# Kernel tuning notes

Hardware: AMD Instinct MI355X
Metric: run time of the kernel (lower is better)

The kernel has to match this reference:

```python
import jax, jax.numpy as jnp
import numpy as np

DIM = 2048
HEADS = 16
HEAD_DIM = DIM // HEADS
B, S = 2, 2048


def setup_inputs() -> dict:
    key = jax.random.key(0)
    k1, k2, k3 = jax.random.split(key, 3)
    x = jax.random.normal(k1, (B, S, DIM), dtype=jnp.float32)
    # causal mask (True = keep), realistic production usage of masked_fill(mask==0,...)
    mask = jnp.tril(jnp.ones((S, S), dtype=bool))
    scale = 1.0 / np.sqrt(DIM)
    W_qkv = jax.random.normal(k2, (DIM, 3 * DIM), dtype=jnp.float32) * scale
    b_qkv = jnp.zeros((3 * DIM,), dtype=jnp.float32)
    W_out = jax.random.normal(k3, (DIM, DIM), dtype=jnp.float32) * scale
    b_out = jnp.zeros((DIM,), dtype=jnp.float32)
    return {"x": x, "mask": mask, "W_qkv": W_qkv, "b_qkv": b_qkv,
            "W_out": W_out, "b_out": b_out}


def reference(x, mask, W_qkv, b_qkv, W_out, b_out):
    b, s, d = x.shape
    # fused QKV projection: [b,s,3d]
    qkv = jnp.einsum('bsd,de->bse', x, W_qkv) + b_qkv
    # [b, s, h, 3*hd] -> [b, h, s, 3*hd] -> chunk into q,k,v
    qkv = qkv.reshape(b, s, HEADS, 3 * HEAD_DIM).transpose(0, 2, 1, 3)
    q, k, v = jnp.split(qkv, 3, axis=-1)  # each [b,h,s,hd]
    scores = jnp.einsum('bhqd,bhkd->bhqk', q, k) / np.sqrt(HEAD_DIM)
    scores = jnp.where(mask, scores, jnp.float32(-1e9))
    attn = jax.nn.softmax(scores, axis=-1)
    # dropout_rate = 0.0 (eval) -> identity
    out = jnp.einsum('bhqk,bhkd->bhqd', attn, v)  # [b,h,s,hd]
    out = out.transpose(0, 2, 1, 3).reshape(b, s, d)
    return jnp.einsum('bsd,de->bse', out, W_out) + b_out
```

## Files before the change

kernel.cpp:

```cpp
#include <hip/hip_runtime.h>
#include <hip/hip_bf16.h>

#define SEQ   2048
#define DIMSZ 2048
#define NHEAD 16
#define HD    128
#define KDIM  2048

typedef __attribute__((ext_vector_type(8))) short bf16x8;
typedef __attribute__((ext_vector_type(4))) float f32x4;
typedef __attribute__((ext_vector_type(4))) short short4v;
typedef __attribute__((ext_vector_type(4))) float float4v;

__device__ __forceinline__ short f2bf(float f) {
    union { __hip_bfloat16 h; short s; } u;
    u.h = __float2bfloat16(f);
    return u.s;
}

__device__ __forceinline__ unsigned pack_bf2(float lo, float hi) {
    return (unsigned)(unsigned short)f2bf(lo) | ((unsigned)(unsigned short)f2bf(hi) << 16);
}

__device__ __forceinline__ void gload_lds16(const void* g, void* l) {
    __builtin_amdgcn_global_load_lds(
        (const __attribute__((address_space(1))) void*)g,
        (__attribute__((address_space(3))) void*)l, 16, 0, 0);
}

__global__ __launch_bounds__(256) void fused_prep(const float* __restrict__ x,
                                                  short* __restrict__ x_bf,
                                                  const float* __restrict__ W_qkv,
                                                  short* __restrict__ wqkv_t,
                                                  const float* __restrict__ W_out,
                                                  short* __restrict__ wout_t) {
    __shared__ float tile[32][33];
    const int bid = blockIdx.x, tid = threadIdx.x;
    if (bid < 8192) {
        int i = (bid * 256 + tid) * 4;
        float4v v = *reinterpret_cast<const float4v*>(x + i);
        short4v o;
        o[0] = f2bf(v[0]); o[1] = f2bf(v[1]); o[2] = f2bf(v[2]); o[3] = f2bf(v[3]);
        *reinterpret_cast<short4v*>(x_bf + i) = o;
        return;
    }
    const float* in;
    short* out;
    int R, C, c0, r0;
    if (bid < 20480) {
        int tb = bid - 8192;
        in = W_qkv; out = wqkv_t; R = 2048; C = 6144;
        c0 = (tb % 192) * 32; r0 = (tb / 192) * 32;
    } else {
        int tb = bid - 20480;
        in = W_out; out = wout_t; R = 2048; C = 2048;
        c0 = (tb % 64) * 32; r0 = (tb / 64) * 32;
    }
    const int tx = tid & 31, ty = tid >> 5;
#pragma unroll
    for (int i = 0; i < 32; i += 8)
        tile[ty + i][tx] = in[(long)(r0 + ty + i) * C + c0 + tx];
    __syncthreads();
#pragma unroll
    for (int i = 0; i < 32; i += 8)
        out[(long)(c0 + ty + i) * R + r0 + tx] = f2bf(tile[tx][ty + i]);
}

template <int MODE, int BM, int BN, int WMC, int WNC>
__global__ __launch_bounds__(512, 2) void gemm8p(const short* __restrict__ A,
                                                 const short* __restrict__ Bt,
                                                 const float* __restrict__ bias,
                                                 float* __restrict__ outf,
                                                 short* __restrict__ q_buf,
                                                 short* __restrict__ k_buf,
                                                 short* __restrict__ vt_buf,
                                                 int ntx) {
    constexpr int QMW = (BM / 2) / WMC;
    constexpr int QNW = (BN / 2) / WNC;
    constexpr int MA = QMW / 16;
    constexpr int NB = QNW / 16;
    constexpr int UA = BM / 64, UB = BN / 64, UT = UA + UB;
    constexpr int RA = MA * 2, RB = NB * 2;
    constexpr int BH0C = (BN / 2 + 63) / 64;
    constexpr int NE = UA / 2 + BH0C, NL = UT - NE;
    constexpr int S0 = 2, S2 = 2;
    constexpr int VM0 = NE + S0;
    constexpr int VM2 = NL + S2;
    constexpr int VM3 = (NE - S2) + NE;
    constexpr int NT = KDIM / 64;

    __shared__ __align__(16) short Alds[2][BM * 64];
    __shared__ __align__(16) short Blds[2][BN * 64];

    const int tid = threadIdx.x;
    const int wv = tid >> 6, ln = tid & 63;
    const int lr = ln & 15, lg = ln >> 4;
    const int wm = wv / WNC, wn = wv % WNC;
    const int q8 = gridDim.x >> 3;
    const int id = blockIdx.x;
    const int swz = (id & 7) * q8 + (id >> 3);
    const int m0 = (swz / ntx) * BM, n0 = (swz % ntx) * BN;

    const int r_l = wv * 8 + (ln >> 3);
    const int g8 = ((ln & 7) ^ ((ln >> 3) & 7)) << 3;

#define STAGE_U(u, bufi, TT)                                                   \
    {                                                                          \
        const bool isA_ = (u) < UA / 2 || (u) >= UA / 2 + UB;                  \
        const int idx_ = (u) < UA / 2 ? (u)                                    \
                         : ((u) < UA / 2 + UB ? (u) - UA / 2 : (u) - UB);      \
        if (isA_)                                                              \
            gload_lds16(A + (long)(m0 + idx_ * 64 + r_l) * KDIM + (TT)*64 + g8,\
                        &Alds[bufi][idx_ * 4096 + wv * 512]);                  \
        else                                                                   \
            gload_lds16(Bt + (long)(n0 + idx_ * 64 + r_l) * KDIM + (TT)*64 + g8,\
                        &Blds[bufi][idx_ * 4096 + wv * 512]);                  \
    }

#define RD(L_, row_, kk_) \
    (*reinterpret_cast<const bf16x8*>(&(L_)[(row_)*64 + ((((kk_)*4 + lg) ^ ((row_)&7)) << 3)]))

#define RD_A(bufi, mh, bank)                                                   \
    _Pragma("unroll") for (int mi = 0; mi < MA; ++mi) {                        \
        int r_ = (mh) * (BM / 2) + wm * QMW + mi * 16 + lr;                    \
        bank[mi][0] = RD(Alds[bufi], r_, 0);                                   \
        bank[mi][1] = RD(Alds[bufi], r_, 1);                                   \
    }
#define RD_B(bufi, nh, bank)                                                   \
    _Pragma("unroll") for (int ni = 0; ni < NB; ++ni) {                        \
        int r_ = (nh) * (BN / 2) + wn * QNW + ni * 16 + lr;                    \
        bank[ni][0] = RD(Blds[bufi], r_, 0);                                   \
        bank[ni][1] = RD(Blds[bufi], r_, 1);                                   \
    }

#define MFMA_Q(qi, AB, BB)                                                     \
    __builtin_amdgcn_s_setprio(1);                                             \
    _Pragma("unroll") for (int kk = 0; kk < 2; ++kk)                           \
        _Pragma("unroll") for (int mi = 0; mi < MA; ++mi)                      \
            _Pragma("unroll") for (int ni = 0; ni < NB; ++ni)                  \
                acc[qi][mi][ni] = __builtin_amdgcn_mfma_f32_16x16x32_bf16(     \
                    AB[mi][kk], BB[ni][kk], acc[qi][mi][ni], 0, 0, 0);         \
    __builtin_amdgcn_s_setprio(0);

#define LGKM(n)                                                                \
    asm volatile("s_waitcnt lgkmcnt(%0)" ::"i"(n) : "memory");                 \
    __builtin_amdgcn_sched_barrier(0);
#define VMC(n) asm volatile("s_waitcnt vmcnt(%0)" ::"i"(n) : "memory");
#define BAR()                                                                  \
    __builtin_amdgcn_s_barrier();                                              \
    __builtin_amdgcn_sched_barrier(0);

    f32x4 acc[4][MA][NB] = {};
    bf16x8 aF0[MA][2], aF1[MA][2], bF0a[NB][2], bF0b[NB][2], bF1[NB][2];

#pragma unroll
    for (int u = 0; u < UT; ++u) STAGE_U(u, 0, 0);
#pragma unroll
    for (int u = 0; u < NE; ++u) STAGE_U(u, 1, 1);
    VMC(NE);
    BAR();
    RD_A(0, 0, aF0);
    RD_B(0, 0, bF0a);

#define TILE_BODY(PAR, T_, BF0C, BF0N)                                         \
    {                                                                          \
        constexpr int cur = PAR, nxt = PAR ^ 1;                                \
        RD_B(cur, 1, bF1);                                                     \
        if ((T_) + 1 < NT) {                                                   \
            STAGE_U(NE + 0, nxt, (T_) + 1);                                    \
            STAGE_U(NE + 1, nxt, (T_) + 1);                                    \
        }                                                                      \
        LGKM(RB);                                                              \
        MFMA_Q(0, aF0, BF0C);                                                  \
        VMC(VM0);                                                              \
        BAR();                                                                 \
        RD_A(cur, 1, aF1);                                                     \
        if ((T_) + 1 < NT) {                                                   \
            _Pragma("unroll") for (int u = NE + S0; u < UT; ++u)               \
                STAGE_U(u, nxt, (T_) + 1);                                     \
        }                                                                      \
        LGKM(RA);                                                              \
        MFMA_Q(1, aF0, bF1);                                                   \
        BAR();                                                                 \
        if ((T_) + 2 < NT) {                                                   \
            STAGE_U(0, cur, (T_) + 2);                                         \
            STAGE_U(1, cur, (T_) + 2);                                         \
        }                                                                      \
        LGKM(0);                                                               \
        MFMA_Q(2, aF1, bF1);                                                   \
        if ((T_) + 2 < NT) { VMC(VM2); } else { VMC(NL); }                     \
        BAR();                                                                 \
        if ((T_) + 1 < NT) {                                                   \
            RD_A(nxt, 0, aF0);                                                 \
            RD_B(nxt, 0, BF0N);                                                \
        }                                                                      \
        if ((T_) + 2 < NT) {                                                   \
            _Pragma("unroll") for (int u = S2; u < NE; ++u)                    \
                STAGE_U(u, cur, (T_) + 2);                                     \
        }                                                                      \
        LGKM(RA + RB);                                                         \
        MFMA_Q(3, aF1, BF0C);                                                  \
        if ((T_) + 2 < NT) { VMC(VM3); } else { VMC(0); }                      \
        BAR();                                                                 \
    }

    for (int TT = 0; TT < NT; TT += 2) {
        TILE_BODY(0, TT, bF0a, bF0b);
        TILE_BODY(1, TT + 1, bF0b, bF0a);
    }

    const int MH[4] = {0, 0, 1, 1}, NHq[4] = {0, 1, 1, 0};
#pragma unroll
    for (int q = 0; q < 4; ++q) {
#pragma unroll
        for (int mi = 0; mi < MA; ++mi) {
#pragma unroll
            for (int ni = 0; ni < NB; ++ni) {
                int col = n0 + NHq[q] * (BN / 2) + wn * QNW + ni * 16 + lr;
                float bv = bias[col];
#pragma unroll
                for (int j = 0; j < 4; ++j) {
                    int row = m0 + MH[q] * (BM / 2) + wm * QMW + mi * 16 + lg * 4 + j;
                    float v = acc[q][mi][ni][j] + bv;
                    if (MODE == 0) {
                        int h = col / (3 * HD);
                        int jj = col - h * (3 * HD);
                        int b = row >> 11, s = row & 2047;
                        int bh = b * NHEAD + h;
                        short sv = f2bf(v);
                        if (jj < HD)
                            q_buf[(bh * SEQ + s) * HD + jj] = sv;
                        else if (jj < 2 * HD)
                            k_buf[(bh * SEQ + s) * HD + (jj - HD)] = sv;
                        else
                            vt_buf[(bh * HD + (jj - 2 * HD)) * SEQ + s] = sv;
                    } else {
                        outf[(long)row * DIMSZ + col] = v;
                    }
                }
            }
        }
    }
#undef STAGE_U
#undef RD
#undef RD_A
#undef RD_B
#undef MFMA_Q
#undef LGKM
#undef VMC
#undef BAR
#undef TILE_BODY
}

__global__ __launch_bounds__(256, 2) void attn_kernel(const short* __restrict__ q_buf,
                                                      const short* __restrict__ k_buf,
                                                      const short* __restrict__ vt_buf,
                                                      short* __restrict__ ao) {
    __shared__ __align__(16) short Klds[2][64 * 128];
    __shared__ __align__(16) short Vlds[2][128 * 64];
    const int tid = threadIdx.x;
    const int wave = tid >> 6, lane = tid & 63;
    const int lr = lane & 15, lg = lane >> 4;
    const int bx = blockIdx.x;
    const int g = bx >> 5;
    const int qt = (g < 8) ? (15 - g) : (g - 8);
    const int bh = bx & 31;
    const int b = bh >> 4, h = bh & 15;
    const int qbase = qt * 128 + wave * 32;
    const float c2 = 0.12752775f;

    bf16x8 qf[2][4];
    {
        const short* qrow = q_buf + ((long)(bh * SEQ + qbase + lr)) * HD;
#pragma unroll
        for (int mi = 0; mi < 2; ++mi)
#pragma unroll
            for (int c = 0; c < 4; ++c)
                qf[mi][c] = *reinterpret_cast<const bf16x8*>(
                    qrow + mi * 16 * HD + c * 32 + lg * 8);
    }
    asm volatile("s_waitcnt vmcnt(0)" ::: "memory");

    const char* kbase = (const char*)(k_buf + (long)bh * SEQ * HD);
    const char* vbase = (const char*)(vt_buf + (long)bh * HD * SEQ);
    const int krow_l = wave * 4 + (lane >> 4);
    const int kcol_l = ((lane & 15) * 16) ^ ((krow_l & 7) << 4);
    const int vrow_l = wave * 8 + (lane >> 3);
    const int vcol_l = ((lane & 7) * 16) ^ ((vrow_l & 7) << 4);

    const int nt = 2 * (qt + 1);
    auto stage = [&](int bufi, int t) {
        const char* ks = kbase + (long)t * 16384 + (long)krow_l * 256 + kcol_l;
        const char* vs = vbase + (long)t * 128 + (long)vrow_l * (SEQ * 2) + vcol_l;
        short* kd = &Klds[bufi][wave * 512];
        short* vd = &Vlds[bufi][wave * 512];
#pragma unroll
        for (int i = 0; i < 4; ++i) {
            gload_lds16(ks + i * 4096, kd + i * 2048);
            gload_lds16(vs + (long)i * 32 * SEQ * 2, vd + i * 2048);
        }
    };

    f32x4 o_acc[2][8] = {};
    float mrow[2] = {-1e30f, -1e30f}, lrow[2] = {0.f, 0.f};

    const int s0 = (lane & 15) | ((lane & 16) << 1);
    const int s1 = s0 + 16;
    const bool hi_ni = (lane & 32) != 0;

    stage(0, 0);
    for (int t = 0; t < nt; ++t) {
        const int cur = t & 1;
        if (t + 1 < nt) {
            stage(cur ^ 1, t + 1);
            asm volatile("s_waitcnt vmcnt(8)" ::: "memory");
        } else {
            asm volatile("s_waitcnt vmcnt(0)" ::: "memory");
        }
        __builtin_amdgcn_s_barrier();
        __builtin_amdgcn_sched_barrier(0);

        const int kv0 = t * 64;
        if (kv0 <= qbase + 31) {
            const short* kl = &Klds[cur][0];
            const short* vl = &Vlds[cur][0];
            bf16x8 kf[4][4];
#pragma unroll
            for (int c = 0; c < 4; ++c)
#pragma unroll
                for (int ni = 0; ni < 4; ++ni)
                    kf[c][ni] = *reinterpret_cast<const bf16x8*>(
                        kl + (((ni * 16 + lr) * 256 +
                               ((c * 64 + lg * 16) ^ ((lr & 7) << 4))) >> 1));
            f32x4 sc[2][4] = {};
            __builtin_amdgcn_s_setprio(1);
#pragma unroll
            for (int c = 0; c < 4; ++c)
#pragma unroll
                for (int mi = 0; mi < 2; ++mi)
#pragma unroll
                    for (int ni = 0; ni < 4; ++ni)
                        sc[mi][ni] = __builtin_amdgcn_mfma_f32_16x16x32_bf16(
                            kf[c][ni], qf[mi][c], sc[mi][ni], 0, 0, 0);
            __builtin_amdgcn_s_setprio(0);
            bf16x8 vfr[2][8];
#pragma unroll
            for (int kc = 0; kc < 2; ++kc)
#pragma unroll
                for (int n = 0; n < 8; ++n)
                    vfr[kc][n] = *reinterpret_cast<const bf16x8*>(
                        vl + (((n * 16 + lr) * 128 +
                               ((kc * 64 + lg * 16) ^ ((lr & 7) << 4))) >> 1));
            const bool full = (kv0 + 63) <= qbase;
            float mx[2];
#pragma unroll
            for (int mi = 0; mi < 2; ++mi) {
                float m_ = -3e38f;
                const int qg = qbase + mi * 16 + lr;
#pragma unroll
                for (int ni = 0; ni < 4; ++ni)
#pragma unroll
                    for (int j = 0; j < 4; ++j) {
                        float v = sc[mi][ni][j] * c2;
                        if (!full && (kv0 + ni * 16 + lg * 4 + j > qg)) v = -1e9f;
                        sc[mi][ni][j] = v;
                        m_ = fmaxf(m_, v);
                    }
                mx[mi] = m_;
            }
#pragma unroll
            for (int mi = 0; mi < 2; ++mi) {
                mx[mi] = fmaxf(mx[mi], __shfl_xor(mx[mi], 16, 64));
                mx[mi] = fmaxf(mx[mi], __shfl_xor(mx[mi], 32, 64));
            }
            float md = fmaxf(mx[0] - mrow[0], mx[1] - mrow[1]);
            if (!__all(md <= 11.5f)) {
#pragma unroll
                for (int mi = 0; mi < 2; ++mi) {
                    float mn = fmaxf(mrow[mi], mx[mi]);
                    float a = exp2f(mrow[mi] - mn);
                    mrow[mi] = mn;
                    lrow[mi] *= a;
#pragma unroll
                    for (int j = 0; j < 4; ++j) {
                        float aj = __shfl(a, (lane & 48) | (lg * 4 + j), 64);
#pragma unroll
                        for (int n = 0; n < 8; ++n)
                            o_acc[mi][n][j] *= aj;
                    }
                }
            }
            unsigned pk[2][4][2];
#pragma unroll
            for (int mi = 0; mi < 2; ++mi) {
                float ps = 0.f;
#pragma unroll
                for (int ni = 0; ni < 4; ++ni) {
#pragma unroll
                    for (int j = 0; j < 4; ++j) {
                        float p = exp2f(sc[mi][ni][j] - mrow[mi]);
                        sc[mi][ni][j] = p;
                        ps += p;
                    }
                    pk[mi][ni][0] = pack_bf2(sc[mi][ni][0], sc[mi][ni][1]);
                    pk[mi][ni][1] = pack_bf2(sc[mi][ni][2], sc[mi][ni][3]);
                }
                lrow[mi] += ps;
            }
#pragma unroll
            for (int kc = 0; kc < 2; ++kc) {
                union { int i[4]; bf16x8 v; } pa[2];
#pragma unroll
                for (int mi = 0; mi < 2; ++mi) {
                    int a0 = __shfl((int)pk[mi][2 * kc][0], s0, 64);
                    int b0 = __shfl((int)pk[mi][2 * kc + 1][0], s0, 64);
                    int a1 = __shfl((int)pk[mi][2 * kc][1], s0, 64);
                    int b1 = __shfl((int)pk[mi][2 * kc + 1][1], s0, 64);
                    int a2 = __shfl((int)pk[mi][2 * kc][0], s1, 64);
                    int b2 = __shfl((int)pk[mi][2 * kc + 1][0], s1, 64);
                    int a3 = __shfl((int)pk[mi][2 * kc][1], s1, 64);
                    int b3 = __shfl((int)pk[mi][2 * kc + 1][1], s1, 64);
                    pa[mi].i[0] = hi_ni ? b0 : a0;
                    pa[mi].i[1] = hi_ni ? b1 : a1;
                    pa[mi].i[2] = hi_ni ? b2 : a2;
                    pa[mi].i[3] = hi_ni ? b3 : a3;
                }
                __builtin_amdgcn_s_setprio(1);
#pragma unroll
                for (int n = 0; n < 8; ++n)
#pragma unroll
                    for (int mi = 0; mi < 2; ++mi)
                        o_acc[mi][n] = __builtin_amdgcn_mfma_f32_16x16x32_bf16(
                            pa[mi].v, vfr[kc][n], o_acc[mi][n], 0, 0, 0);
                __builtin_amdgcn_s_setprio(0);
            }
        }
        __builtin_amdgcn_s_barrier();
    }

    float invq[2];
#pragma unroll
    for (int mi = 0; mi < 2; ++mi) {
        float s = lrow[mi];
        s += __shfl_xor(s, 16, 64);
        s += __shfl_xor(s, 32, 64);
        invq[mi] = 1.0f / s;
    }
    short* aor = ao + ((long)(b * SEQ + qbase) * DIMSZ + h * HD);
#pragma unroll
    for (int mi = 0; mi < 2; ++mi)
#pragma unroll
        for (int j = 0; j < 4; ++j) {
            float ij = __shfl(invq[mi], (lane & 48) | (lg * 4 + j), 64);
#pragma unroll
            for (int n = 0; n < 8; ++n)
                aor[(mi * 16 + lg * 4 + j) * DIMSZ + n * 16 + lr] =
                    f2bf(o_acc[mi][n][j] * ij);
        }
}

extern "C" void kernel_launch(void* const* d_in, const int* in_sizes, int n_in,
                              void* d_out, int out_size, void* d_ws, size_t ws_size,
                              hipStream_t stream) {
    const float* x     = (const float*)d_in[0];
    const float* W_qkv = (const float*)d_in[2];
    const float* b_qkv = (const float*)d_in[3];
    const float* W_out = (const float*)d_in[4];
    const float* b_out = (const float*)d_in[5];
    float* out = (float*)d_out;

    char* ws = (char*)d_ws;
    short* x_bf   = (short*)ws;
    short* wqkv_t = (short*)(ws + (size_t)16 * 1048576);
    short* wout_t = (short*)(ws + (size_t)40 * 1048576);
    short* q_buf  = (short*)(ws + (size_t)48 * 1048576);
    short* k_buf  = (short*)(ws + (size_t)64 * 1048576);
    short* vt_buf = (short*)(ws + (size_t)80 * 1048576);
    short* ao     = x_bf;

    fused_prep<<<24576, 256, 0, stream>>>(x, x_bf, W_qkv, wqkv_t, W_out, wout_t);
    gemm8p<0, 256, 192, 4, 2><<<512, 512, 0, stream>>>(x_bf, wqkv_t, b_qkv, nullptr,
                                                       q_buf, k_buf, vt_buf, 32);
    attn_kernel<<<512, 256, 0, stream>>>(q_buf, k_buf, vt_buf, ao);
    gemm8p<1, 128, 256, 2, 4><<<256, 512, 0, stream>>>(ao, wout_t, b_out, out,
                                                       nullptr, nullptr, nullptr, 8);
}
```

Baseline: 286.7 us.

## Shrink attention blocks to two waves with 32-key KV tiles

Restructures the causal attention kernel so each block covers 64 query rows with 2 waves instead of 128 rows with 4 waves, and streams K/V in 32-key tiles instead of 64. The grid doubles to 1024 blocks, the LDS double buffers halve, and the QK^T and PV loops are rebuilt around the smaller tile, with K fragments now loaded per chunk. The aim is less LDS and register pressure, higher occupancy and finer load balance across the causal triangle. The cost is that K/V data is reused by fewer query rows, so global and LDS traffic per query rises, and there are more barrier and softmax-rescale steps per row.

```diff
diff --git a/kernel.cpp b/kernel.cpp
--- a/kernel.cpp
+++ b/kernel.cpp
@@ -252,21 +252,21 @@
 #undef TILE_BODY
 }
 
-__global__ __launch_bounds__(256, 2) void attn_kernel(const short* __restrict__ q_buf,
+__global__ __launch_bounds__(128, 2) void attn_kernel(const short* __restrict__ q_buf,
                                                       const short* __restrict__ k_buf,
                                                       const short* __restrict__ vt_buf,
                                                       short* __restrict__ ao) {
-    __shared__ __align__(16) short Klds[2][64 * 128];
-    __shared__ __align__(16) short Vlds[2][128 * 64];
+    __shared__ __align__(16) short Klds[2][32 * 128];
+    __shared__ __align__(16) short Vlds[2][128 * 32];
     const int tid = threadIdx.x;
     const int wave = tid >> 6, lane = tid & 63;
     const int lr = lane & 15, lg = lane >> 4;
     const int bx = blockIdx.x;
     const int g = bx >> 5;
-    const int qt = (g < 8) ? (15 - g) : (g - 8);
+    const int qt = (g < 16) ? (31 - g) : (g - 16);
     const int bh = bx & 31;
     const int b = bh >> 4, h = bh & 15;
-    const int qbase = qt * 128 + wave * 32;
+    const int qbase = qt * 64 + wave * 32;
     const float c2 = 0.12752775f;
 
     bf16x8 qf[2][4];
@@ -285,19 +285,19 @@
     const char* vbase = (const char*)(vt_buf + (long)bh * HD * SEQ);
     const int krow_l = wave * 4 + (lane >> 4);
     const int kcol_l = ((lane & 15) * 16) ^ ((krow_l & 7) << 4);
-    const int vrow_l = wave * 8 + (lane >> 3);
-    const int vcol_l = ((lane & 7) * 16) ^ ((vrow_l & 7) << 4);
+    const int vrow_l = wave * 16 + (lane >> 2);
+    const int vcol_l = ((lane & 3) * 16) ^ (((lane >> 2) & 3) << 4);
 
     const int nt = 2 * (qt + 1);
     auto stage = [&](int bufi, int t) {
-        const char* ks = kbase + (long)t * 16384 + (long)krow_l * 256 + kcol_l;
-        const char* vs = vbase + (long)t * 128 + (long)vrow_l * (SEQ * 2) + vcol_l;
+        const char* ks = kbase + (long)t * 8192 + (long)krow_l * 256 + kcol_l;
+        const char* vs = vbase + (long)t * 64 + (long)vrow_l * (SEQ * 2) + vcol_l;
         short* kd = &Klds[bufi][wave * 512];
         short* vd = &Vlds[bufi][wave * 512];
 #pragma unroll
         for (int i = 0; i < 4; ++i) {
-            gload_lds16(ks + i * 4096, kd + i * 2048);
-            gload_lds16(vs + (long)i * 32 * SEQ * 2, vd + i * 2048);
+            gload_lds16(ks + i * 2048, kd + i * 1024);
+            gload_lds16(vs + (long)i * 32 * (SEQ * 2), vd + i * 1024);
         }
     };
 
@@ -320,45 +320,41 @@
         __builtin_amdgcn_s_barrier();
         __builtin_amdgcn_sched_barrier(0);
 
-        const int kv0 = t * 64;
+        const int kv0 = t * 32;
         if (kv0 <= qbase + 31) {
             const short* kl = &Klds[cur][0];
             const short* vl = &Vlds[cur][0];
-            bf16x8 kf[4][4];
-#pragma unroll
-            for (int c = 0; c < 4; ++c)
-#pragma unroll
-                for (int ni = 0; ni < 4; ++ni)
-                    kf[c][ni] = *reinterpret_cast<const bf16x8*>(
+            f32x4 sc[2][2] = {};
+#pragma unroll
+            for (int c = 0; c < 4; ++c) {
+                bf16x8 kf[2];
+#pragma unroll
+                for (int ni = 0; ni < 2; ++ni)
+                    kf[ni] = *reinterpret_cast<const bf16x8*>(
                         kl + (((ni * 16 + lr) * 256 +
                                ((c * 64 + lg * 16) ^ ((lr & 7) << 4))) >> 1));
-            f32x4 sc[2][4] = {};
-            __builtin_amdgcn_s_setprio(1);
-#pragma unroll
-            for (int c = 0; c < 4; ++c)
+                __builtin_amdgcn_s_setprio(1);
 #pragma unroll
                 for (int mi = 0; mi < 2; ++mi)
 #pragma unroll
-                    for (int ni = 0; ni < 4; ++ni)
+                    for (int ni = 0; ni < 2; ++ni)
                         sc[mi][ni] = __builtin_amdgcn_mfma_f32_16x16x32_bf16(
-                            kf[c][ni], qf[mi][c], sc[mi][ni], 0, 0, 0);
-            __builtin_amdgcn_s_setprio(0);
-            bf16x8 vfr[2][8];
-#pragma unroll
-            for (int kc = 0; kc < 2; ++kc)
-#pragma unroll
-                for (int n = 0; n < 8; ++n)
-                    vfr[kc][n] = *reinterpret_cast<const bf16x8*>(
-                        vl + (((n * 16 + lr) * 128 +
-                               ((kc * 64 + lg * 16) ^ ((lr & 7) << 4))) >> 1));
-            const bool full = (kv0 + 63) <= qbase;
+                            kf[ni], qf[mi][c], sc[mi][ni], 0, 0, 0);
+                __builtin_amdgcn_s_setprio(0);
+            }
+            bf16x8 vfr[8];
+#pragma unroll
+            for (int n = 0; n < 8; ++n)
+                vfr[n] = *reinterpret_cast<const bf16x8*>(
+                    vl + (((n * 16 + lr) * 32) + (((lg ^ (lr & 3)) << 4) >> 1)));
+            const bool full = (kv0 + 31) <= qbase;
             float mx[2];
 #pragma unroll
             for (int mi = 0; mi < 2; ++mi) {
                 float m_ = -3e38f;
                 const int qg = qbase + mi * 16 + lr;
 #pragma unroll
-                for (int ni = 0; ni < 4; ++ni)
+                for (int ni = 0; ni < 2; ++ni)
 #pragma unroll
                     for (int j = 0; j < 4; ++j) {
                         float v = sc[mi][ni][j] * c2;
@@ -390,12 +386,12 @@
                     }
                 }
             }
-            unsigned pk[2][4][2];
+            unsigned pk[2][2][2];
 #pragma unroll
             for (int mi = 0; mi < 2; ++mi) {
                 float ps = 0.f;
 #pragma unroll
-                for (int ni = 0; ni < 4; ++ni) {
+                for (int ni = 0; ni < 2; ++ni) {
 #pragma unroll
                     for (int j = 0; j < 4; ++j) {
                         float p = exp2f(sc[mi][ni][j] - mrow[mi]);
@@ -407,33 +403,30 @@
                 }
                 lrow[mi] += ps;
             }
-#pragma unroll
-            for (int kc = 0; kc < 2; ++kc) {
-                union { int i[4]; bf16x8 v; } pa[2];
-#pragma unroll
-                for (int mi = 0; mi < 2; ++mi) {
-                    int a0 = __shfl((int)pk[mi][2 * kc][0], s0, 64);
-                    int b0 = __shfl((int)pk[mi][2 * kc + 1][0], s0, 64);
-                    int a1 = __shfl((int)pk[mi][2 * kc][1], s0, 64);
-                    int b1 = __shfl((int)pk[mi][2 * kc + 1][1], s0, 64);
-                    int a2 = __shfl((int)pk[mi][2 * kc][0], s1, 64);
-                    int b2 = __shfl((int)pk[mi][2 * kc + 1][0], s1, 64);
-                    int a3 = __shfl((int)pk[mi][2 * kc][1], s1, 64);
-                    int b3 = __shfl((int)pk[mi][2 * kc + 1][1], s1, 64);
-                    pa[mi].i[0] = hi_ni ? b0 : a0;
-                    pa[mi].i[1] = hi_ni ? b1 : a1;
-                    pa[mi].i[2] = hi_ni ? b2 : a2;
-                    pa[mi].i[3] = hi_ni ? b3 : a3;
-                }
-                __builtin_amdgcn_s_setprio(1);
-#pragma unroll
-                for (int n = 0; n < 8; ++n)
-#pragma unroll
-                    for (int mi = 0; mi < 2; ++mi)
-                        o_acc[mi][n] = __builtin_amdgcn_mfma_f32_16x16x32_bf16(
-                            pa[mi].v, vfr[kc][n], o_acc[mi][n], 0, 0, 0);
-                __builtin_amdgcn_s_setprio(0);
-            }
+            union { int i[4]; bf16x8 v; } pa[2];
+#pragma unroll
+            for (int mi = 0; mi < 2; ++mi) {
+                int a0 = __shfl((int)pk[mi][0][0], s0, 64);
+                int b0 = __shfl((int)pk[mi][1][0], s0, 64);
+                int a1 = __shfl((int)pk[mi][0][1], s0, 64);
+                int b1 = __shfl((int)pk[mi][1][1], s0, 64);
+                int a2 = __shfl((int)pk[mi][0][0], s1, 64);
+                int b2 = __shfl((int)pk[mi][1][0], s1, 64);
+                int a3 = __shfl((int)pk[mi][0][1], s1, 64);
+                int b3 = __shfl((int)pk[mi][1][1], s1, 64);
+                pa[mi].i[0] = hi_ni ? b0 : a0;
+                pa[mi].i[1] = hi_ni ? b1 : a1;
+                pa[mi].i[2] = hi_ni ? b2 : a2;
+                pa[mi].i[3] = hi_ni ? b3 : a3;
+            }
+            __builtin_amdgcn_s_setprio(1);
+#pragma unroll
+            for (int n = 0; n < 8; ++n)
+#pragma unroll
+                for (int mi = 0; mi < 2; ++mi)
+                    o_acc[mi][n] = __builtin_amdgcn_mfma_f32_16x16x32_bf16(
+                        pa[mi].v, vfr[n], o_acc[mi][n], 0, 0, 0);
+            __builtin_amdgcn_s_setprio(0);
         }
         __builtin_amdgcn_s_barrier();
     }
@@ -481,7 +474,7 @@
     fused_prep<<<24576, 256, 0, stream>>>(x, x_bf, W_qkv, wqkv_t, W_out, wout_t);
     gemm8p<0, 256, 192, 4, 2><<<512, 512, 0, stream>>>(x_bf, wqkv_t, b_qkv, nullptr,
                                                        q_buf, k_buf, vt_buf, 32);
-    attn_kernel<<<512, 256, 0, stream>>>(q_buf, k_buf, vt_buf, ao);
+    attn_kernel<<<1024, 128, 0, stream>>>(q_buf, k_buf, vt_buf, ao);
     gemm8p<1, 128, 256, 2, 4><<<256, 512, 0, stream>>>(ao, wout_t, b_out, out,
                                                        nullptr, nullptr, nullptr, 8);
 }
```

Measured after the change: 302.5 us. 5.5% more time.
